# Optimization experiments

Hardware: AMD Instinct MI355X
Metric: run time of the kernel (lower is better)

The kernel has to match this reference:

```python
import jax, jax.numpy as jnp
import numpy as np

B, D, S, U, H = 2, 1024, 2048, 1024, 16
LN_EPS = 1e-5

def setup_inputs() -> dict:
    key = jax.random.key(0)
    ks = jax.random.split(key, 5)
    std = 0.02
    return {
        "inputs": jax.random.normal(ks[0], (B, D, S), jnp.float32),
        "Wq": jax.random.normal(ks[1], (D, U), jnp.float32) * std,
        "bq": jnp.zeros((U,), jnp.float32),
        "Wk": jax.random.normal(ks[2], (D, U), jnp.float32) * std,
        "bk": jnp.zeros((U,), jnp.float32),
        "Wv": jax.random.normal(ks[3], (D, U), jnp.float32) * std,
        "bv": jnp.zeros((U,), jnp.float32),
        "Wo": jax.random.normal(ks[4], (U, D), jnp.float32) * std,
        "bo": jnp.zeros((D,), jnp.float32),
        "gamma": jnp.ones((D,), jnp.float32),
        "beta": jnp.zeros((D,), jnp.float32),
        "num_heads": H,
    }

def reference(inputs, Wq, bq, Wk, bk, Wv, bv, Wo, bo, gamma, beta, num_heads):
    # inputs: (B, D, S) -> (B, S, D)
    x = jnp.transpose(inputs, (0, 2, 1))
    b, s, d = x.shape

    def proj(W, bias):
        y = jax.nn.relu(x @ W + bias)               # (b, s, U)
        y = y.reshape(b, s, num_heads, -1)
        return jnp.transpose(y, (0, 2, 1, 3))       # (b, h, s, hd)

    Q = proj(Wq, bq)
    K = proj(Wk, bk)
    V = proj(Wv, bv)
    hd = Q.shape[-1]
    scale = 1.0 / np.sqrt(hd).astype(np.float32)

    # Block-wise flash attention in the source is mathematically plain softmax attention
    # (per-block epsilon 1e-10 is negligible); scale applied to Q, no mask, no dropout.
    scores = jnp.einsum('bhid,bhjd->bhij', Q * scale, K)   # (b, h, s, s)
    P = jax.nn.softmax(scores, axis=-1)
    O = jnp.einsum('bhij,bhjd->bhid', P, V)                # (b, h, s, hd)

    O = jnp.transpose(O, (0, 2, 1, 3)).reshape(b, s, -1)   # (b, s, U)
    out = O @ Wo + bo + x                                  # residual add
    mean = jnp.mean(out, axis=-1, keepdims=True)
    var = jnp.var(out, axis=-1, keepdims=True)
    y = (out - mean) * jax.lax.rsqrt(var + LN_EPS) * gamma + beta
    return jnp.transpose(y, (0, 2, 1))                     # (B, D, S)
```

## Files before the change

### kernel.cpp

```cpp
#include <hip/hip_runtime.h>
#include <hip/hip_bf16.h>

typedef __bf16 bf16x8 __attribute__((ext_vector_type(8)));
typedef __bf16 bf16x4 __attribute__((ext_vector_type(4)));
typedef float  f32x4  __attribute__((ext_vector_type(4)));
typedef float  f32x16 __attribute__((ext_vector_type(16)));

#define MFMA16(a, b, c) __builtin_amdgcn_mfma_f32_16x16x32_bf16((a), (b), (c), 0, 0, 0)
#define MFMA32(a, b, c) __builtin_amdgcn_mfma_f32_32x32x16_bf16((a), (b), (c), 0, 0, 0)

namespace {
constexpr int Bb = 2, Dd = 1024, Ss = 2048, Uu = 1024, Hh = 16;
}

#if __has_builtin(__builtin_amdgcn_exp2f)
#define EXP2(x) __builtin_amdgcn_exp2f(x)
#else
#define EXP2(x) __expf((x) * 0.6931471805599453f)
#endif

__device__ __forceinline__ uint32_t pkbf(float a, float b) {
  union { __bf16 h[2]; uint32_t u; } z;
  z.h[0] = (__bf16)a; z.h[1] = (__bf16)b;
  return z.u;
}
#define PLSWAP(a, b) asm("v_permlane32_swap_b32 %0, %1" : "+v"(a), "+v"(b))

__device__ __forceinline__ void gl16(const void* g, void* l) {
  __builtin_amdgcn_global_load_lds((const __attribute__((address_space(1))) uint32_t*)g,
                                   (__attribute__((address_space(3))) uint32_t*)l, 16, 0, 0);
}

#define VMW(n) asm volatile("s_waitcnt vmcnt(" #n ")" ::: "memory")
#define BARRIER_PIN() do { __builtin_amdgcn_s_barrier(); \
  asm volatile("" ::: "memory"); __builtin_amdgcn_sched_barrier(0); } while (0)
#define LGKM0() asm volatile("s_waitcnt lgkmcnt(0)" ::: "memory")

__global__ __launch_bounds__(256) void k_xpose_x(const float* __restrict__ inp,
                                                 __bf16* __restrict__ xb, float* __restrict__ xt) {
  __shared__ __attribute__((aligned(16))) float xs[64][65];
  const int s0 = blockIdx.x * 64, d0 = blockIdx.y * 64, b = blockIdx.z;
  const int t = threadIdx.x;
  {
    const int i = t >> 2, c = (t & 3) * 16;
    const float* src = inp + ((size_t)(b * Dd + d0 + i)) * Ss + s0 + c;
#pragma unroll
    for (int q = 0; q < 4; ++q) {
      const float4 f = *(const float4*)(src + q * 4);
      xs[i][c + q * 4 + 0] = f.x; xs[i][c + q * 4 + 1] = f.y;
      xs[i][c + q * 4 + 2] = f.z; xs[i][c + q * 4 + 3] = f.w;
    }
  }
  __syncthreads();
  {
    const int sl = t >> 2, dc = (t & 3) * 16;
    float* dstf = xt + ((size_t)(b * Ss + s0 + sl)) * Dd + d0 + dc;
    bf16x8 va, vb;
#pragma unroll
    for (int q = 0; q < 4; ++q) {
      float4 f;
      f.x = xs[dc + q * 4 + 0][sl]; f.y = xs[dc + q * 4 + 1][sl];
      f.z = xs[dc + q * 4 + 2][sl]; f.w = xs[dc + q * 4 + 3][sl];
      *(float4*)(dstf + q * 4) = f;
    }
#pragma unroll
    for (int j = 0; j < 8; ++j) { va[j] = (__bf16)xs[dc + j][sl]; vb[j] = (__bf16)xs[dc + 8 + j][sl]; }
    __bf16* dst = xb + ((size_t)(b * Ss + s0 + sl)) * Dd + d0 + dc;
    *(bf16x8*)dst = va;
    *(bf16x8*)(dst + 8) = vb;
  }
}

__global__ __launch_bounds__(256) void k_xpose_w(const float* __restrict__ w0, const float* __restrict__ w1,
                                                 const float* __restrict__ w2, const float* __restrict__ w3,
                                                 __bf16* __restrict__ o0, __bf16* __restrict__ o1,
                                                 __bf16* __restrict__ o2, __bf16* __restrict__ o3) {
  __shared__ __attribute__((aligned(16))) __bf16 ts[64][72];
  const float* src_m; __bf16* dst_m;
  switch (blockIdx.z) {
    case 0: src_m = w0; dst_m = o0; break;
    case 1: src_m = w1; dst_m = o1; break;
    case 2: src_m = w2; dst_m = o2; break;
    default: src_m = w3; dst_m = o3; break;
  }
  const int n0 = blockIdx.x * 64, k0 = blockIdx.y * 64;
  const int t = threadIdx.x;
  {
    const int i = t >> 2, c = (t & 3) * 16;
    const float* src = src_m + (size_t)(k0 + i) * 1024 + n0 + c;
#pragma unroll
    for (int q = 0; q < 4; ++q) {
      const float4 f = *(const float4*)(src + q * 4);
      ts[i][c + q * 4 + 0] = (__bf16)f.x;
      ts[i][c + q * 4 + 1] = (__bf16)f.y;
      ts[i][c + q * 4 + 2] = (__bf16)f.z;
      ts[i][c + q * 4 + 3] = (__bf16)f.w;
    }
  }
  __syncthreads();
  {
    const int nl = t >> 2, kc = (t & 3) * 16;
    bf16x8 va, vb;
#pragma unroll
    for (int j = 0; j < 8; ++j) { va[j] = ts[kc + j][nl]; vb[j] = ts[kc + 8 + j][nl]; }
    __bf16* dst = dst_m + (size_t)(n0 + nl) * 1024 + k0 + kc;
    *(bf16x8*)dst = va;
    *(bf16x8*)(dst + 8) = vb;
  }
}

__device__ __forceinline__ int swz_slot(int row, int slot) { return (slot + (row >> 1)) & 3; }

__device__ __forceinline__ void gemm_core(const __bf16* __restrict__ A, const __bf16* __restrict__ Bt,
                                          __bf16 (*__restrict__ As)[128][32], __bf16 (*__restrict__ Bs)[128][32],
                                          int m0, int n0, int t, f32x4 acc[4][4]) {
  const int w = t >> 6, l = t & 63;
  const int wm = (w >> 1) * 64, wn = (w & 1) * 64;
  const int lg = l >> 4, lr = l & 15;
  const int sr = t >> 2, sc8 = t & 3;
  const int so = ((sc8 + 4 - ((sr >> 1) & 3)) & 3) * 8;
  const __bf16* ga = A + (size_t)(m0 + sr) * 1024 + so;
  const __bf16* gb = Bt + (size_t)(n0 + sr) * 1024 + so;
  const int de = sr * 32 + sc8 * 8;
#define STG(bf, kk) { \
    gl16(ga + (kk) * 32,             &As[bf][0][0] + de); \
    gl16(ga + (kk) * 32 + 64 * 1024, &As[bf][0][0] + de + 64 * 32); \
    gl16(gb + (kk) * 32,             &Bs[bf][0][0] + de); \
    gl16(gb + (kk) * 32 + 64 * 1024, &Bs[bf][0][0] + de + 64 * 32); }
  STG(0, 0) STG(1, 1)
  for (int s = 0; s < 32; ++s) {
    if (s < 31) { VMW(4); } else { VMW(0); }
    BARRIER_PIN();
    if (s + 2 < 32) { const int b2 = (s + 2) % 3; STG(b2, s + 2) }
    const int cb = s % 3;
    bf16x8 af[4], bfr[4];
#pragma unroll
    for (int i = 0; i < 4; ++i) { const int rr = wm + i * 16 + lr; af[i]  = *(const bf16x8*)&As[cb][rr][swz_slot(rr, lg) * 8]; }
#pragma unroll
    for (int i = 0; i < 4; ++i) { const int rr = wn + i * 16 + lr; bfr[i] = *(const bf16x8*)&Bs[cb][rr][swz_slot(rr, lg) * 8]; }
#pragma unroll
    for (int i = 0; i < 4; ++i)
#pragma unroll
      for (int j = 0; j < 4; ++j) acc[i][j] = MFMA16(af[i], bfr[j], acc[i][j]);
  }
#undef STG
}

__device__ __forceinline__ void epi_qk(f32x4 acc[4][4], const float* bias, __bf16* out,
                                       int m0, int n0, int t, float scale) {
  const int w = t >> 6, l = t & 63;
  const int wm = (w >> 1) * 64, wn = (w & 1) * 64;
  const int lg = l >> 4, lr = l & 15;
  const int b = m0 >> 11;
  const int sbase = (m0 & 2047) + wm + lg * 4;
#pragma unroll
  for (int j = 0; j < 4; ++j) {
    const int n = n0 + wn + j * 16 + lr;
    const float bi = bias[n];
    const int h = n >> 6, e = n & 63;
    __bf16* obase = out + ((size_t)(b * Hh + h) * Ss) * 64 + e;
#pragma unroll
    for (int i = 0; i < 4; ++i)
#pragma unroll
      for (int r = 0; r < 4; ++r) {
        const int s = sbase + i * 16 + r;
        float v = acc[i][j][r] + bi;
        v = fmaxf(v, 0.0f) * scale;
        obase[(size_t)s * 64] = (__bf16)v;
      }
  }
}

__device__ __forceinline__ void epi_vt(f32x4 acc[4][4], const float* bias, __bf16* out,
                                       int m0, int n0, int t) {
  const int w = t >> 6, l = t & 63;
  const int wm = (w >> 1) * 64, wn = (w & 1) * 64;
  const int lg = l >> 4, lr = l & 15;
  const int b = m0 >> 11;
  const int sb = (m0 & 2047) + wm + lg * 4;
#pragma unroll
  for (int j = 0; j < 4; ++j) {
    const int n = n0 + wn + j * 16 + lr;
    const float bi = bias[n];
    __bf16* obase = out + (size_t)(b * 1024 + n) * Ss + sb;
#pragma unroll
    for (int i = 0; i < 4; ++i) {
      bf16x4 z;
#pragma unroll
      for (int r = 0; r < 4; ++r) z[r] = (__bf16)fmaxf(acc[i][j][r] + bi, 0.0f);
      *(bf16x4*)(obase + i * 16) = z;
    }
  }
}

__global__ __launch_bounds__(256) void k_gemm_qkv(const __bf16* __restrict__ A,
    const __bf16* __restrict__ W0, const __bf16* __restrict__ W1, const __bf16* __restrict__ W2,
    const float* __restrict__ b0, const float* __restrict__ b1, const float* __restrict__ b2,
    __bf16* __restrict__ Qb, __bf16* __restrict__ Kb, __bf16* __restrict__ Vt) {
  __shared__ __attribute__((aligned(16))) __bf16 As[3][128][32];
  __shared__ __attribute__((aligned(16))) __bf16 Bs[3][128][32];
  const int flat = blockIdx.x;
  const int logical = (flat & 7) * 96 + (flat >> 3);
  const int z = logical >> 8;
  const int rem = logical & 255;
  const int n0 = (rem & 7) * 128, m0 = (rem >> 3) * 128;
  const __bf16* Bt = (z == 0) ? W0 : (z == 1) ? W1 : W2;
  const float* bias = (z == 0) ? b0 : (z == 1) ? b1 : b2;
  const int t = threadIdx.x;
  f32x4 acc[4][4] = {};
  gemm_core(A, Bt, As, Bs, m0, n0, t, acc);
  if (z == 0) epi_qk(acc, bias, Qb, m0, n0, t, 0.125f * 1.44269504f);
  else if (z == 1) epi_qk(acc, bias, Kb, m0, n0, t, 1.0f);
  else epi_vt(acc, bias, Vt, m0, n0, t);
}

__global__ __launch_bounds__(256) void k_gemm_o(const __bf16* __restrict__ A, const __bf16* __restrict__ Bt,
                                                const float* __restrict__ bias, const float* __restrict__ xt,
                                                float* __restrict__ Wb, float* __restrict__ partials) {
  __shared__ __attribute__((aligned(16))) __bf16 As[3][128][32];
  __shared__ __attribute__((aligned(16))) __bf16 Bs[3][128][32];
  const int flat = blockIdx.x;
  const int logical = (flat & 7) * 32 + (flat >> 3);
  const int n0 = (logical & 7) * 128, m0 = (logical >> 3) * 128;
  const int t = threadIdx.x, w = t >> 6, l = t & 63;
  const int wm = (w >> 1) * 64, wn = (w & 1) * 64;
  const int lg = l >> 4, lr = l & 15;
  f32x4 acc[4][4] = {};
  gemm_core(A, Bt, As, Bs, m0, n0, t, acc);
  float rs[4][4], rq[4][4];
#pragma unroll
  for (int i = 0; i < 4; ++i)
#pragma unroll
    for (int r = 0; r < 4; ++r) { rs[i][r] = 0.f; rq[i][r] = 0.f; }
#pragma unroll
  for (int j = 0; j < 4; ++j) {
    const int n = n0 + wn + j * 16 + lr;
    const float bi = bias[n];
#pragma unroll
    for (int i = 0; i < 4; ++i)
#pragma unroll
      for (int r = 0; r < 4; ++r) {
        const int m = m0 + wm + i * 16 + lg * 4 + r;
        const float v = acc[i][j][r] + bi + xt[(size_t)m * 1024 + n];
        Wb[(size_t)m * 1024 + n] = v;
        rs[i][r] += v; rq[i][r] += v * v;
      }
  }
  const int ci = (n0 + wn) >> 6;
#pragma unroll
  for (int i = 0; i < 4; ++i)
#pragma unroll
    for (int r = 0; r < 4; ++r) {
      float s = rs[i][r], q = rq[i][r];
      s += __shfl_xor(s, 1); s += __shfl_xor(s, 2); s += __shfl_xor(s, 4); s += __shfl_xor(s, 8);
      q += __shfl_xor(q, 1); q += __shfl_xor(q, 2); q += __shfl_xor(q, 4); q += __shfl_xor(q, 8);
      if (lr == 0) {
        const int m = m0 + wm + i * 16 + lg * 4 + r;
        partials[((size_t)m * 16 + ci) * 2]     = s;
        partials[((size_t)m * 16 + ci) * 2 + 1] = q;
      }
    }
}

__global__ __launch_bounds__(256, 2) void k_attn5(const __bf16* __restrict__ Qg, const __bf16* __restrict__ Kg,
                                                  const __bf16* __restrict__ Vt, __bf16* __restrict__ Og) {
  __shared__ __attribute__((aligned(16))) __bf16 Ks[2][64][72];
  __shared__ __attribute__((aligned(16))) __bf16 Vs[2][64][72];
  const int t = threadIdx.x, l = t & 63, w = t >> 6;
  const int ln = l & 31, hi = l >> 5;
  const int bid = blockIdx.x;
  const int orig = (bid & 7) * 64 + (bid >> 3);
  const int bh = orig >> 4, qt = orig & 15;
  const int q0w = qt * 128 + w * 32;
  const int b = bh >> 4, h = bh & 15;
  const size_t kbase = (size_t)bh * Ss * 64;
  const int srow = t >> 2, scol = (t & 3) * 16;
  const __bf16* Krow = Kg + kbase + (size_t)srow * 64 + scol;
  const __bf16* Vrow = Vt + (size_t)(bh * 64 + srow) * Ss + scol;

  bf16x8 qf0, qf1, qf2, qf3;
  {
    const __bf16* qp = Qg + kbase + (size_t)(q0w + ln) * 64 + hi * 8;
    qf0 = *(const bf16x8*)(qp);
    qf1 = *(const bf16x8*)(qp + 16);
    qf2 = *(const bf16x8*)(qp + 32);
    qf3 = *(const bf16x8*)(qp + 48);
  }
  f32x16 oA = {}, oB = {};
  float lrow = 0.f;

  auto tile_compute = [&](const __bf16 (&K)[64][72], const __bf16 (&V)[64][72]) {
    f32x16 s0 = {}, s1 = {};
    {
      bf16x8 kf;
#define QK(u, cc, sacc) \
      kf = *(const bf16x8*)&K[(u) * 32 + ln][(cc) * 16 + hi * 8]; \
      sacc = MFMA32(kf, qf##cc, sacc);
      QK(0, 0, s0) QK(0, 1, s0) QK(0, 2, s0) QK(0, 3, s0)
      QK(1, 0, s1) QK(1, 1, s1) QK(1, 2, s1) QK(1, 3, s1)
#undef QK
    }
#pragma unroll
    for (int r = 0; r < 16; ++r) s0[r] = EXP2(s0[r]);
#pragma unroll
    for (int r = 0; r < 16; ++r) s1[r] = EXP2(s1[r]);
    float sm[16];
#pragma unroll
    for (int r = 0; r < 8; ++r) sm[r] = s0[2 * r] + s0[2 * r + 1];
#pragma unroll
    for (int r = 0; r < 8; ++r) sm[8 + r] = s1[2 * r] + s1[2 * r + 1];
#pragma unroll
    for (int st = 8; st > 0; st >>= 1)
#pragma unroll
      for (int r = 0; r < st; ++r) sm[r] += sm[r + st];
    lrow += sm[0];
    uint32_t w0[8], w1[8];
#pragma unroll
    for (int k = 0; k < 8; ++k) w0[k] = pkbf(s0[2 * k], s0[2 * k + 1]);
#pragma unroll
    for (int k = 0; k < 8; ++k) w1[k] = pkbf(s1[2 * k], s1[2 * k + 1]);
    PLSWAP(w0[0], w0[2]); PLSWAP(w0[1], w0[3]);
    PLSWAP(w0[4], w0[6]); PLSWAP(w0[5], w0[7]);
    PLSWAP(w1[0], w1[2]); PLSWAP(w1[1], w1[3]);
    PLSWAP(w1[4], w1[6]); PLSWAP(w1[5], w1[7]);
    union U4 { uint32_t u[4]; bf16x8 v; };
    U4 z;
    bf16x8 pa0, pa1, pa2, pa3;
    z.u[0] = w0[0]; z.u[1] = w0[1]; z.u[2] = w0[2]; z.u[3] = w0[3]; pa0 = z.v;
    z.u[0] = w0[4]; z.u[1] = w0[5]; z.u[2] = w0[6]; z.u[3] = w0[7]; pa1 = z.v;
    z.u[0] = w1[0]; z.u[1] = w1[1]; z.u[2] = w1[2]; z.u[3] = w1[3]; pa2 = z.v;
    z.u[0] = w1[4]; z.u[1] = w1[5]; z.u[2] = w1[6]; z.u[3] = w1[7]; pa3 = z.v;
    {
      bf16x8 vf;
#define PV(half, ti, pa, oacc) \
      vf = *(const bf16x8*)&V[(half) * 32 + ln][(ti) * 16 + hi * 8]; \
      oacc = MFMA32(vf, pa, oacc);
      PV(0, 0, pa0, oA) PV(0, 1, pa1, oA) PV(0, 2, pa2, oA) PV(0, 3, pa3, oA)
      PV(1, 0, pa0, oB) PV(1, 1, pa1, oB) PV(1, 2, pa2, oB) PV(1, 3, pa3, oB)
#undef PV
    }
  };

  bf16x8 kA0 = *(const bf16x8*)(Krow),      kA1 = *(const bf16x8*)(Krow + 8);
  bf16x8 vA0 = *(const bf16x8*)(Vrow),      vA1 = *(const bf16x8*)(Vrow + 8);
  bf16x8 kB0 = *(const bf16x8*)(Krow + 64 * 64), kB1 = *(const bf16x8*)(Krow + 64 * 64 + 8);
  bf16x8 vB0 = *(const bf16x8*)(Vrow + 64), vB1 = *(const bf16x8*)(Vrow + 64 + 8);

  for (int tt = 0; tt < 16; ++tt) {
    *(bf16x8*)&Ks[0][srow][scol]     = kA0;
    *(bf16x8*)&Ks[0][srow][scol + 8] = kA1;
    *(bf16x8*)&Vs[0][srow][scol]     = vA0;
    *(bf16x8*)&Vs[0][srow][scol + 8] = vA1;
    LGKM0();
    BARRIER_PIN();
    if (tt < 15) {
      const size_t ko = (size_t)(2 * tt + 2) * 64;
      kA0 = *(const bf16x8*)(Krow + ko * 64);
      kA1 = *(const bf16x8*)(Krow + ko * 64 + 8);
      vA0 = *(const bf16x8*)(Vrow + ko);
      vA1 = *(const bf16x8*)(Vrow + ko + 8);
    }
    tile_compute(Ks[0], Vs[0]);
    *(bf16x8*)&Ks[1][srow][scol]     = kB0;
    *(bf16x8*)&Ks[1][srow][scol + 8] = kB1;
    *(bf16x8*)&Vs[1][srow][scol]     = vB0;
    *(bf16x8*)&Vs[1][srow][scol + 8] = vB1;
    LGKM0();
    BARRIER_PIN();
    if (tt < 15) {
      const size_t ko = (size_t)(2 * tt + 3) * 64;
      kB0 = *(const bf16x8*)(Krow + ko * 64);
      kB1 = *(const bf16x8*)(Krow + ko * 64 + 8);
      vB0 = *(const bf16x8*)(Vrow + ko);
      vB1 = *(const bf16x8*)(Vrow + ko + 8);
    }
    tile_compute(Ks[1], Vs[1]);
  }
  {
    uint32_t a = __builtin_bit_cast(uint32_t, lrow), bsw = a;
    PLSWAP(a, bsw);
    lrow = __builtin_bit_cast(float, a) + __builtin_bit_cast(float, bsw);
  }
  const float rl = 1.0f / lrow;
  __bf16* ob = Og + ((size_t)(b * Ss + q0w + ln)) * Uu + h * 64 + hi * 4;
#pragma unroll
  for (int r0 = 0; r0 < 4; ++r0) {
    bf16x4 z0, z1;
#pragma unroll
    for (int j = 0; j < 4; ++j) z0[j] = (__bf16)(oA[r0 * 4 + j] * rl);
#pragma unroll
    for (int j = 0; j < 4; ++j) z1[j] = (__bf16)(oB[r0 * 4 + j] * rl);
    *(bf16x4*)(ob + r0 * 8) = z0;
    *(bf16x4*)(ob + 32 + r0 * 8) = z1;
  }
}

__global__ __launch_bounds__(256) void k_ln_stats(const float* __restrict__ partials, float* __restrict__ stats) {
  const int row = blockIdx.x * 256 + threadIdx.x;
  float s = 0.f, q = 0.f;
#pragma unroll
  for (int c = 0; c < 16; ++c) {
    s += partials[((size_t)row * 16 + c) * 2];
    q += partials[((size_t)row * 16 + c) * 2 + 1];
  }
  const float mean = s * (1.0f / 1024.0f);
  const float var = q * (1.0f / 1024.0f) - mean * mean;
  stats[row * 2] = mean;
  stats[row * 2 + 1] = rsqrtf(var + 1e-5f);
}

__global__ __launch_bounds__(256) void k_ln_write(const float* __restrict__ Wb, const float* __restrict__ stats,
                                                  const float* __restrict__ gamma, const float* __restrict__ beta,
                                                  float* __restrict__ out) {
  __shared__ __attribute__((aligned(16))) float ws0[64][65];
  __shared__ float sm[64][2];
  const int d0 = blockIdx.x * 64, s0 = blockIdx.y * 64, b = blockIdx.z;
  const int t = threadIdx.x;
  {
    const int sl = t >> 2, dc = (t & 3) * 16;
    const float* src = Wb + ((size_t)(b * Ss + s0 + sl)) * Dd + d0 + dc;
#pragma unroll
    for (int q = 0; q < 4; ++q) {
      const float4 f = *(const float4*)(src + q * 4);
      ws0[dc + q * 4 + 0][sl] = f.x; ws0[dc + q * 4 + 1][sl] = f.y;
      ws0[dc + q * 4 + 2][sl] = f.z; ws0[dc + q * 4 + 3][sl] = f.w;
    }
  }
  if (t < 128) sm[t >> 1][t & 1] = stats[(size_t)(b * Ss + s0 + (t >> 1)) * 2 + (t & 1)];
  __syncthreads();
  const int dl = t >> 2, sc = (t & 3) * 16;
  const float g = gamma[d0 + dl], be = beta[d0 + dl];
  float* dst = out + ((size_t)(b * Dd + d0 + dl)) * Ss + s0 + sc;
#pragma unroll
  for (int q = 0; q < 4; ++q) {
    float4 o;
    o.x = (ws0[dl][sc + q * 4 + 0] - sm[sc + q * 4 + 0][0]) * sm[sc + q * 4 + 0][1] * g + be;
    o.y = (ws0[dl][sc + q * 4 + 1] - sm[sc + q * 4 + 1][0]) * sm[sc + q * 4 + 1][1] * g + be;
    o.z = (ws0[dl][sc + q * 4 + 2] - sm[sc + q * 4 + 2][0]) * sm[sc + q * 4 + 2][1] * g + be;
    o.w = (ws0[dl][sc + q * 4 + 3] - sm[sc + q * 4 + 3][0]) * sm[sc + q * 4 + 3][1] * g + be;
    *(float4*)(dst + q * 4) = o;
  }
}

extern "C" void kernel_launch(void* const* d_in, const int* in_sizes, int n_in,
                              void* d_out, int out_size, void* d_ws, size_t ws_size,
                              hipStream_t stream) {
  const float* inp   = (const float*)d_in[0];
  const float* Wq    = (const float*)d_in[1];
  const float* bq    = (const float*)d_in[2];
  const float* Wk    = (const float*)d_in[3];
  const float* bk    = (const float*)d_in[4];
  const float* Wv    = (const float*)d_in[5];
  const float* bv    = (const float*)d_in[6];
  const float* Wo    = (const float*)d_in[7];
  const float* bo    = (const float*)d_in[8];
  const float* gamma = (const float*)d_in[9];
  const float* beta  = (const float*)d_in[10];

  char* ws = (char*)d_ws;
  const size_t MB = 1ull << 20;
  __bf16* xb  = (__bf16*)(ws);
  __bf16* Wqt = (__bf16*)(ws + 8 * MB);
  __bf16* Wkt = (__bf16*)(ws + 10 * MB);
  __bf16* Wvt = (__bf16*)(ws + 12 * MB);
  __bf16* Wot = (__bf16*)(ws + 14 * MB);
  __bf16* Qb  = (__bf16*)(ws + 16 * MB);
  __bf16* Kb  = (__bf16*)(ws + 24 * MB);
  __bf16* Vtb = (__bf16*)(ws + 32 * MB);
  __bf16* Ob  = (__bf16*)(ws + 40 * MB);
  float*  xt  = (float*)(ws + 48 * MB);
  float*  Wb  = (float*)(ws + 16 * MB);
  float*  partials = (float*)(ws + 8 * MB);
  float*  stats    = (float*)(ws + 8 * MB + 512 * 1024);

  k_xpose_x<<<dim3(32, 16, 2), 256, 0, stream>>>(inp, xb, xt);
  k_xpose_w<<<dim3(16, 16, 4), 256, 0, stream>>>(Wq, Wk, Wv, Wo, Wqt, Wkt, Wvt, Wot);
  k_gemm_qkv<<<dim3(768), 256, 0, stream>>>(xb, Wqt, Wkt, Wvt, bq, bk, bv, Qb, Kb, Vtb);
  k_attn5<<<dim3(512), 256, 0, stream>>>(Qb, Kb, Vtb, Ob);
  k_gemm_o<<<dim3(256), 256, 0, stream>>>(Ob, Wot, bo, xt, Wb, partials);
  k_ln_stats<<<dim3(16), 256, 0, stream>>>(partials, stats);
  k_ln_write<<<dim3(16, 32, 2), 256, 0, stream>>>(Wb, stats, gamma, beta, (float*)d_out);
}
```

Before: 162.7 us.

## Stage GEMM and attention epilogues through shared memory for coalesced stores

The QKV GEMM, O-projection GEMM and attention kernels now write their accumulator tiles into shared memory (aliased over the operand staging buffers) and then store to global memory with wide, row-contiguous vector writes. The old epilogues issued scattered 2-byte or strided stores. The O-projection epilogue now also reads the residual with float4 loads and computes the LayerNorm partial sums from those coalesced rows. The cost is extra barriers and LDS traffic per tile, plus possible bank conflicts in the scalar LDS writes.

```diff
diff --git a/kernel.cpp b/kernel.cpp
--- a/kernel.cpp
+++ b/kernel.cpp
@@ -146,50 +146,62 @@
 #undef STG
 }
 
-__device__ __forceinline__ void epi_qk(f32x4 acc[4][4], const float* bias, __bf16* out,
-                                       int m0, int n0, int t, float scale) {
+__device__ __forceinline__ void epi_qk_c(f32x4 acc[4][4], const float* bias, __bf16* out,
+                                         int m0, int n0, int t, float scale, __bf16* Ct) {
   const int w = t >> 6, l = t & 63;
   const int wm = (w >> 1) * 64, wn = (w & 1) * 64;
   const int lg = l >> 4, lr = l & 15;
-  const int b = m0 >> 11;
-  const int sbase = (m0 & 2047) + wm + lg * 4;
+  __syncthreads();
 #pragma unroll
   for (int j = 0; j < 4; ++j) {
-    const int n = n0 + wn + j * 16 + lr;
-    const float bi = bias[n];
-    const int h = n >> 6, e = n & 63;
-    __bf16* obase = out + ((size_t)(b * Hh + h) * Ss) * 64 + e;
+    const int nl = wn + j * 16 + lr;
+    const float bi = bias[n0 + nl];
 #pragma unroll
     for (int i = 0; i < 4; ++i)
 #pragma unroll
       for (int r = 0; r < 4; ++r) {
-        const int s = sbase + i * 16 + r;
-        float v = acc[i][j][r] + bi;
-        v = fmaxf(v, 0.0f) * scale;
-        obase[(size_t)s * 64] = (__bf16)v;
+        const int ml = wm + i * 16 + lg * 4 + r;
+        Ct[ml * 132 + nl] = (__bf16)(fmaxf(acc[i][j][r] + bi, 0.0f) * scale);
       }
   }
-}
-
-__device__ __forceinline__ void epi_vt(f32x4 acc[4][4], const float* bias, __bf16* out,
-                                       int m0, int n0, int t) {
+  __syncthreads();
+  const int b = m0 >> 11, h0 = n0 >> 6, sb = m0 & 2047;
+  const int sub = t & 7, rid0 = t >> 3;
+#pragma unroll
+  for (int p = 0; p < 8; ++p) {
+    const int rid = p * 32 + rid0;
+    const int sl = rid & 127, hh = rid >> 7;
+    const bf16x8 v = *(const bf16x8*)&Ct[sl * 132 + hh * 64 + sub * 8];
+    *(bf16x8*)(out + ((size_t)(b * Hh + h0 + hh) * Ss + sb + sl) * 64 + sub * 8) = v;
+  }
+}
+
+__device__ __forceinline__ void epi_vt_c(f32x4 acc[4][4], const float* bias, __bf16* out,
+                                         int m0, int n0, int t, __bf16* Ct) {
   const int w = t >> 6, l = t & 63;
   const int wm = (w >> 1) * 64, wn = (w & 1) * 64;
   const int lg = l >> 4, lr = l & 15;
-  const int b = m0 >> 11;
-  const int sb = (m0 & 2047) + wm + lg * 4;
+  __syncthreads();
 #pragma unroll
   for (int j = 0; j < 4; ++j) {
-    const int n = n0 + wn + j * 16 + lr;
-    const float bi = bias[n];
-    __bf16* obase = out + (size_t)(b * 1024 + n) * Ss + sb;
-#pragma unroll
-    for (int i = 0; i < 4; ++i) {
-      bf16x4 z;
-#pragma unroll
-      for (int r = 0; r < 4; ++r) z[r] = (__bf16)fmaxf(acc[i][j][r] + bi, 0.0f);
-      *(bf16x4*)(obase + i * 16) = z;
-    }
+    const int nl = wn + j * 16 + lr;
+    const float bi = bias[n0 + nl];
+#pragma unroll
+    for (int i = 0; i < 4; ++i)
+#pragma unroll
+      for (int r = 0; r < 4; ++r) {
+        const int ml = wm + i * 16 + lg * 4 + r;
+        Ct[nl * 132 + ml] = (__bf16)fmaxf(acc[i][j][r] + bi, 0.0f);
+      }
+  }
+  __syncthreads();
+  const int b = m0 >> 11, sb = m0 & 2047;
+  const int sub = t & 15, rid0 = t >> 4;
+#pragma unroll
+  for (int p = 0; p < 8; ++p) {
+    const int rid = p * 16 + rid0;
+    const bf16x8 v = *(const bf16x8*)&Ct[rid * 132 + sub * 8];
+    *(bf16x8*)(out + (size_t)(b * 1024 + n0 + rid) * Ss + sb + sub * 8) = v;
   }
 }
 
@@ -197,8 +209,10 @@
     const __bf16* __restrict__ W0, const __bf16* __restrict__ W1, const __bf16* __restrict__ W2,
     const float* __restrict__ b0, const float* __restrict__ b1, const float* __restrict__ b2,
     __bf16* __restrict__ Qb, __bf16* __restrict__ Kb, __bf16* __restrict__ Vt) {
-  __shared__ __attribute__((aligned(16))) __bf16 As[3][128][32];
-  __shared__ __attribute__((aligned(16))) __bf16 Bs[3][128][32];
+  __shared__ __attribute__((aligned(16))) char smem[49152];
+  auto As = (__bf16 (*)[128][32])smem;
+  auto Bs = (__bf16 (*)[128][32])(smem + 24576);
+  __bf16* Ct = (__bf16*)smem;
   const int flat = blockIdx.x;
   const int logical = (flat & 7) * 96 + (flat >> 3);
   const int z = logical >> 8;
@@ -209,16 +223,18 @@
   const int t = threadIdx.x;
   f32x4 acc[4][4] = {};
   gemm_core(A, Bt, As, Bs, m0, n0, t, acc);
-  if (z == 0) epi_qk(acc, bias, Qb, m0, n0, t, 0.125f * 1.44269504f);
-  else if (z == 1) epi_qk(acc, bias, Kb, m0, n0, t, 1.0f);
-  else epi_vt(acc, bias, Vt, m0, n0, t);
+  if (z == 0) epi_qk_c(acc, bias, Qb, m0, n0, t, 0.125f * 1.44269504f, Ct);
+  else if (z == 1) epi_qk_c(acc, bias, Kb, m0, n0, t, 1.0f, Ct);
+  else epi_vt_c(acc, bias, Vt, m0, n0, t, Ct);
 }
 
 __global__ __launch_bounds__(256) void k_gemm_o(const __bf16* __restrict__ A, const __bf16* __restrict__ Bt,
                                                 const float* __restrict__ bias, const float* __restrict__ xt,
                                                 float* __restrict__ Wb, float* __restrict__ partials) {
-  __shared__ __attribute__((aligned(16))) __bf16 As[3][128][32];
-  __shared__ __attribute__((aligned(16))) __bf16 Bs[3][128][32];
+  __shared__ __attribute__((aligned(16))) char smem[49152];
+  auto As = (__bf16 (*)[128][32])smem;
+  auto Bs = (__bf16 (*)[128][32])(smem + 24576);
+  float* Cs = (float*)smem;
   const int flat = blockIdx.x;
   const int logical = (flat & 7) * 32 + (flat >> 3);
   const int n0 = (logical & 7) * 128, m0 = (logical >> 3) * 128;
@@ -227,51 +243,57 @@
   const int lg = l >> 4, lr = l & 15;
   f32x4 acc[4][4] = {};
   gemm_core(A, Bt, As, Bs, m0, n0, t, acc);
-  float rs[4][4], rq[4][4];
-#pragma unroll
-  for (int i = 0; i < 4; ++i)
-#pragma unroll
-    for (int r = 0; r < 4; ++r) { rs[i][r] = 0.f; rq[i][r] = 0.f; }
-#pragma unroll
-  for (int j = 0; j < 4; ++j) {
-    const int n = n0 + wn + j * 16 + lr;
-    const float bi = bias[n];
-#pragma unroll
-    for (int i = 0; i < 4; ++i)
-#pragma unroll
-      for (int r = 0; r < 4; ++r) {
-        const int m = m0 + wm + i * 16 + lg * 4 + r;
-        const float v = acc[i][j][r] + bi + xt[(size_t)m * 1024 + n];
-        Wb[(size_t)m * 1024 + n] = v;
-        rs[i][r] += v; rq[i][r] += v * v;
+  const int sub = t & 31, rid0 = t >> 5;
+#pragma unroll
+  for (int h2 = 0; h2 < 2; ++h2) {
+    __syncthreads();
+    if ((w >> 1) == h2) {
+#pragma unroll
+      for (int j = 0; j < 4; ++j) {
+        const int nl = wn + j * 16 + lr;
+        const float bi = bias[n0 + nl];
+#pragma unroll
+        for (int i = 0; i < 4; ++i)
+#pragma unroll
+          for (int r = 0; r < 4; ++r)
+            Cs[(i * 16 + lg * 4 + r) * 132 + nl] = acc[i][j][r] + bi;
       }
-  }
-  const int ci = (n0 + wn) >> 6;
-#pragma unroll
-  for (int i = 0; i < 4; ++i)
-#pragma unroll
-    for (int r = 0; r < 4; ++r) {
-      float s = rs[i][r], q = rq[i][r];
+    }
+    __syncthreads();
+#pragma unroll
+    for (int p = 0; p < 8; ++p) {
+      const int row = p * 8 + rid0;
+      const int m = m0 + h2 * 64 + row;
+      float4 v = *(const float4*)&Cs[row * 132 + sub * 4];
+      const float4 x4 = *(const float4*)&xt[(size_t)m * 1024 + n0 + sub * 4];
+      v.x += x4.x; v.y += x4.y; v.z += x4.z; v.w += x4.w;
+      *(float4*)&Wb[(size_t)m * 1024 + n0 + sub * 4] = v;
+      float s = v.x + v.y + v.z + v.w;
+      float q = v.x * v.x + v.y * v.y + v.z * v.z + v.w * v.w;
       s += __shfl_xor(s, 1); s += __shfl_xor(s, 2); s += __shfl_xor(s, 4); s += __shfl_xor(s, 8);
       q += __shfl_xor(q, 1); q += __shfl_xor(q, 2); q += __shfl_xor(q, 4); q += __shfl_xor(q, 8);
-      if (lr == 0) {
-        const int m = m0 + wm + i * 16 + lg * 4 + r;
+      if ((sub & 15) == 0) {
+        const int ci = (n0 >> 6) + (sub >> 4);
         partials[((size_t)m * 16 + ci) * 2]     = s;
         partials[((size_t)m * 16 + ci) * 2 + 1] = q;
       }
     }
-}
-
-__global__ __launch_bounds__(256, 2) void k_attn5(const __bf16* __restrict__ Qg, const __bf16* __restrict__ Kg,
+  }
+}
+
+__global__ __launch_bounds__(256, 2) void k_attn6(const __bf16* __restrict__ Qg, const __bf16* __restrict__ Kg,
                                                   const __bf16* __restrict__ Vt, __bf16* __restrict__ Og) {
-  __shared__ __attribute__((aligned(16))) __bf16 Ks[2][64][72];
-  __shared__ __attribute__((aligned(16))) __bf16 Vs[2][64][72];
+  __shared__ __attribute__((aligned(16))) char smem[36864];
+  auto Ks = (__bf16 (*)[64][72])smem;
+  auto Vs = (__bf16 (*)[64][72])(smem + 18432);
+  __bf16* Os = (__bf16*)smem;
   const int t = threadIdx.x, l = t & 63, w = t >> 6;
   const int ln = l & 31, hi = l >> 5;
   const int bid = blockIdx.x;
   const int orig = (bid & 7) * 64 + (bid >> 3);
   const int bh = orig >> 4, qt = orig & 15;
-  const int q0w = qt * 128 + w * 32;
+  const int q0blk = qt * 128;
+  const int q0w = q0blk + w * 32;
   const int b = bh >> 4, h = bh & 15;
   const size_t kbase = (size_t)bh * Ss * 64;
   const int srow = t >> 2, scol = (t & 3) * 16;
@@ -382,16 +404,22 @@
     lrow = __builtin_bit_cast(float, a) + __builtin_bit_cast(float, bsw);
   }
   const float rl = 1.0f / lrow;
-  __bf16* ob = Og + ((size_t)(b * Ss + q0w + ln)) * Uu + h * 64 + hi * 4;
-#pragma unroll
-  for (int r0 = 0; r0 < 4; ++r0) {
-    bf16x4 z0, z1;
-#pragma unroll
-    for (int j = 0; j < 4; ++j) z0[j] = (__bf16)(oA[r0 * 4 + j] * rl);
-#pragma unroll
-    for (int j = 0; j < 4; ++j) z1[j] = (__bf16)(oB[r0 * 4 + j] * rl);
-    *(bf16x4*)(ob + r0 * 8) = z0;
-    *(bf16x4*)(ob + 32 + r0 * 8) = z1;
+  __syncthreads();
+  const int ql = w * 32 + ln;
+#pragma unroll
+  for (int r0 = 0; r0 < 4; ++r0)
+#pragma unroll
+    for (int j = 0; j < 4; ++j) {
+      Os[ql * 68 + hi * 4 + r0 * 8 + j]      = (__bf16)(oA[r0 * 4 + j] * rl);
+      Os[ql * 68 + 32 + hi * 4 + r0 * 8 + j] = (__bf16)(oB[r0 * 4 + j] * rl);
+    }
+  __syncthreads();
+  const int sub = t & 7, rid0 = t >> 3;
+#pragma unroll
+  for (int p = 0; p < 4; ++p) {
+    const int rid = p * 32 + rid0;
+    const bf16x8 v = *(const bf16x8*)&Os[rid * 68 + sub * 8];
+    *(bf16x8*)(Og + ((size_t)(b * Ss + q0blk + rid)) * Uu + h * 64 + sub * 8) = v;
   }
 }
 
@@ -476,7 +504,7 @@
   k_xpose_x<<<dim3(32, 16, 2), 256, 0, stream>>>(inp, xb, xt);
   k_xpose_w<<<dim3(16, 16, 4), 256, 0, stream>>>(Wq, Wk, Wv, Wo, Wqt, Wkt, Wvt, Wot);
   k_gemm_qkv<<<dim3(768), 256, 0, stream>>>(xb, Wqt, Wkt, Wvt, bq, bk, bv, Qb, Kb, Vtb);
-  k_attn5<<<dim3(512), 256, 0, stream>>>(Qb, Kb, Vtb, Ob);
+  k_attn6<<<dim3(512), 256, 0, stream>>>(Qb, Kb, Vtb, Ob);
   k_gemm_o<<<dim3(256), 256, 0, stream>>>(Ob, Wot, bo, xt, Wb, partials);
   k_ln_stats<<<dim3(16), 256, 0, stream>>>(partials, stats);
   k_ln_write<<<dim3(16, 32, 2), 256, 0, stream>>>(Wb, stats, gamma, beta, (float*)d_out);
```

Result: faster. 145.4 us (-10.6%).
